# Kernel optimization log

Measured on AMD Instinct MI355X. Metric: run time of the kernel, lower is better.

## Reference

```python
import jax, jax.numpy as jnp
import numpy as np

C = 256

def setup_inputs() -> dict:
    key = jax.random.key(0)
    ks = jax.random.split(key, 8)
    B, H, W = 4, 64, 64
    x = jax.random.normal(ks[0], (B, C, H, W), dtype=jnp.float32)
    # 1x1 conv weights ~ kaiming uniform; bias zero
    bound = np.sqrt(6.0 / C)
    Wq = jax.random.uniform(ks[1], (C, C), minval=-bound, maxval=bound, dtype=jnp.float32)
    Wk = jax.random.uniform(ks[2], (C, C), minval=-bound, maxval=bound, dtype=jnp.float32)
    Wv = jax.random.uniform(ks[3], (C, C), minval=-bound, maxval=bound, dtype=jnp.float32)
    bq = jnp.zeros((C,), jnp.float32)
    bk = jnp.zeros((C,), jnp.float32)
    bv = jnp.zeros((C,), jnp.float32)
    # gamma initialized to zero in torch; use small nonzero so output depends on attn path
    gamma = jnp.array([0.1], dtype=jnp.float32)
    return {"x": x, "Wq": Wq, "bq": bq, "Wk": Wk, "bk": bk, "Wv": Wv, "bv": bv, "gamma": gamma}


def reference(x, Wq, bq, Wk, bk, Wv, bv, gamma):
    B, Cc, H, W = x.shape
    N = H * W
    xf = x.reshape(B, Cc, N)  # [B,C,N]
    # 1x1 conv == per-pixel linear over channels: out[b,o,n] = sum_c W[o,c]*x[b,c,n] + b[o]
    q = jnp.einsum('oc,bcn->bon', Wq, xf) + bq[None, :, None]  # [B,C,N]
    k = jnp.einsum('oc,bcn->bon', Wk, xf) + bk[None, :, None]
    v = jnp.einsum('oc,bcn->bon', Wv, xf) + bv[None, :, None]
    # energy[b,i,j] = q[b,:,i] . k[b,:,j]  (no scaling, as in source)
    energy = jnp.einsum('bci,bcj->bij', q, k)  # [B,N,N]
    attention = jax.nn.softmax(energy, axis=-1)
    # out[b,c,i] = sum_j v[b,c,j] * attention[b,i,j]  (bmm(value, attn^T))
    out = jnp.einsum('bcj,bij->bci', v, attention)
    out = out.reshape(B, Cc, H, W)
    return gamma * out + x
```

## Files before the change

### kernel.cpp

```cpp
#include <hip/hip_runtime.h>
#include <hip/hip_bf16.h>
#include <cstdint>


#define C_DIM 256
#define N_DIM 4096
#define B_DIM 4

typedef _Float16 f16;
typedef f16 f16x8 __attribute__((ext_vector_type(8)));
typedef f16 f16x4 __attribute__((ext_vector_type(4)));
typedef float f32x4 __attribute__((ext_vector_type(4)));

__device__ __forceinline__ void dma16(const f16* g, f16* l) {
  __builtin_amdgcn_global_load_lds(
      (const __attribute__((address_space(1))) unsigned int*)g,
      (__attribute__((address_space(3))) unsigned int*)l, 16, 0, 0);
}

__global__ __launch_bounds__(256) void k_prep_xs(const float* __restrict__ x,
                                                 f16* __restrict__ xs) {
  __shared__ float tile[64][65];
  const int b = blockIdx.z, nb = blockIdx.x * 64, cb = blockIdx.y * 64;
  const float* xb = x + (size_t)b * C_DIM * N_DIM;
  for (int i = threadIdx.x; i < 64 * 64; i += 256) {
    int c = i >> 6, n = i & 63;
    tile[c][n] = xb[(size_t)(cb + c) * N_DIM + nb + n];
  }
  __syncthreads();
  f16* xsb = xs + (size_t)b * N_DIM * C_DIM;
  for (int i = threadIdx.x; i < 64 * 64; i += 256) {
    int n = i >> 6, c = i & 63;
    xsb[(size_t)(nb + n) * C_DIM + cb + c] = (f16)tile[c][n];
  }
}

__global__ __launch_bounds__(256) void k_cast_w(const float* __restrict__ Wq,
                                                const float* __restrict__ Wk,
                                                const float* __restrict__ Wv,
                                                f16* __restrict__ Wh) {
  int i = blockIdx.x * 256 + threadIdx.x;
  int sel = i >> 16, j = i & 65535;
  const float* s = (sel == 0) ? Wq : (sel == 1) ? Wk : Wv;
  Wh[i] = (f16)s[j];
}

__global__ __launch_bounds__(256) void k_proj(const f16* __restrict__ xs,
                                              const f16* __restrict__ Wh,
                                              const float* __restrict__ bq,
                                              const float* __restrict__ bk,
                                              const float* __restrict__ bv,
                                              f16* __restrict__ Qh,
                                              f16* __restrict__ Kh,
                                              f16* __restrict__ Vh) {
  const int z = blockIdx.y;
  const int w = threadIdx.x >> 6, lane = threadIdx.x & 63;
  const int quad = lane >> 4, li = lane & 15;
  const f16* W = Wh + (size_t)z * 65536;
  const float* bias = (z == 0) ? bq : (z == 1) ? bk : bv;

  if (z < 2) {
    f16* out = (z == 0) ? Qh : Kh;
    const int g0 = (blockIdx.x * 4 + w) * 16;
    f16x8 a[8];
    const f16* arow = xs + (size_t)(g0 + li) * C_DIM + quad * 8;
#pragma unroll
    for (int kf = 0; kf < 8; kf++) a[kf] = *(const f16x8*)(arow + kf * 32);
    for (int ot = 0; ot < 16; ot++) {
      f32x4 acc = {0.f, 0.f, 0.f, 0.f};
      const f16* brow = W + (size_t)(ot * 16 + li) * C_DIM + quad * 8;
#pragma unroll
      for (int kf = 0; kf < 8; kf++) {
        f16x8 bf = *(const f16x8*)(brow + kf * 32);
        acc = __builtin_amdgcn_mfma_f32_16x16x32_f16(a[kf], bf, acc, 0, 0, 0);
      }
      float bb = bias[ot * 16 + li];
      f16* orow = out + (size_t)g0 * C_DIM + ot * 16 + li;
#pragma unroll
      for (int r = 0; r < 4; r++)
        orow[(size_t)(quad * 4 + r) * C_DIM] = (f16)(acc[r] + bb);
    }
  } else {
    const int t = blockIdx.x * 4 + w;
    const int b = t >> 8, j0 = (t & 255) * 16;
    f16x8 bfr[8];
    const f16* brow = xs + (size_t)(b * N_DIM + j0 + li) * C_DIM + quad * 8;
#pragma unroll
    for (int kf = 0; kf < 8; kf++) bfr[kf] = *(const f16x8*)(brow + kf * 32);
    for (int ot = 0; ot < 16; ot++) {
      f32x4 acc = {0.f, 0.f, 0.f, 0.f};
      const f16* arow = W + (size_t)(ot * 16 + li) * C_DIM + quad * 8;
#pragma unroll
      for (int kf = 0; kf < 8; kf++) {
        f16x8 af = *(const f16x8*)(arow + kf * 32);
        acc = __builtin_amdgcn_mfma_f32_16x16x32_f16(af, bfr[kf], acc, 0, 0, 0);
      }
      f16* obase = Vh + ((size_t)(b * C_DIM + ot * 16 + quad * 4)) * N_DIM + j0 + li;
#pragma unroll
      for (int r = 0; r < 4; r++) {
        float bb = bias[ot * 16 + quad * 4 + r];
        obase[(size_t)r * N_DIM] = (f16)(acc[r] + bb);
      }
    }
  }
}

#define JT 64
#define NT (N_DIM / JT)
#define KBUF 16896
#define VBUF 16896
#define K0_OFF 0
#define K1_OFF 16896
#define V0_OFF 33792
#define V1_OFF 50688
#define P_OFF  67584
#define PSTR 80
#define SMEM_F16 72704

__global__ __launch_bounds__(256, 1) void k_attn(const f16* __restrict__ Qh,
                                                 const f16* __restrict__ Kh,
                                                 const f16* __restrict__ Vh,
                                                 const float* __restrict__ x,
                                                 const float* __restrict__ gamma_p,
                                                 float* __restrict__ out) {
  __shared__ __align__(16) f16 smem[SMEM_F16];
  const int b = blockIdx.y;
  const int tid = threadIdx.x;
  const int w = tid >> 6, lane = tid & 63;
  const int quad = lane >> 4, li = lane & 15;
  const int ibase = blockIdx.x * 64 + w * 16;

  f16x8 qf[8];
  {
    const f16* qrow = Qh + (size_t)(b * N_DIM + ibase + li) * C_DIM + quad * 8;
#pragma unroll
    for (int kf = 0; kf < 8; kf++) qf[kf] = *(const f16x8*)(qrow + kf * 32);
  }
  const f16* Kb = Kh + (size_t)b * N_DIM * C_DIM;
  const f16* Vb = Vh + (size_t)b * C_DIM * N_DIM;
  f16* Pw = smem + P_OFF + w * 16 * PSTR;

  const float LOG2E = 1.4426950408889634f;
  float m = -3.0e38f, l = 0.0f;
  f32x4 acc[16];
#pragma unroll
  for (int ct = 0; ct < 16; ct++) acc[ct] = (f32x4){0.f, 0.f, 0.f, 0.f};

  {
    const f16* kg = Kb;
    const f16* vg = Vb;
#pragma unroll
    for (int it = 0; it < 8; it++) {
      int p = w * 8 + it;
      dma16(kg + (size_t)(2 * p + (lane >> 5)) * C_DIM + (lane & 31) * 8,
            smem + K0_OFF + p * 528);
      dma16(vg + (size_t)(p * 8 + (lane >> 3)) * N_DIM + (lane & 7) * 8,
            smem + V0_OFF + p * 528);
    }
  }
  __syncthreads();

  for (int t = 0; t < NT; t++) {
    const f16* Kc = smem + ((t & 1) ? K1_OFF : K0_OFF);
    const f16* Vc = smem + ((t & 1) ? V1_OFF : V0_OFF);

    if (t + 1 < NT) {
      f16* Kn = smem + ((t & 1) ? K0_OFF : K1_OFF);
      f16* Vn = smem + ((t & 1) ? V0_OFF : V1_OFF);
      const int jt = (t + 1) * JT;
      const f16* kg = Kb + (size_t)jt * C_DIM;
      const f16* vg = Vb + jt;
#pragma unroll
      for (int it = 0; it < 8; it++) {
        int p = w * 8 + it;
        dma16(kg + (size_t)(2 * p + (lane >> 5)) * C_DIM + (lane & 31) * 8,
              Kn + p * 528);
        dma16(vg + (size_t)(p * 8 + (lane >> 3)) * N_DIM + (lane & 7) * 8,
              Vn + p * 528);
      }
    }

    f32x4 s[4];
#pragma unroll
    for (int sub = 0; sub < 4; sub++) {
      f32x4 ss = {0.f, 0.f, 0.f, 0.f};
      const int r = sub * 16 + li;
      const f16* krow = Kc + (r >> 1) * 528 + (r & 1) * 256 + quad * 8;
#pragma unroll
      for (int kf = 0; kf < 8; kf++) {
        f16x8 kfr = *(const f16x8*)(krow + kf * 32);
        ss = __builtin_amdgcn_mfma_f32_16x16x32_f16(kfr, qf[kf], ss, 0, 0, 0);
      }
      s[sub] = ss;
    }

    float tm = -3.0e38f;
#pragma unroll
    for (int sub = 0; sub < 4; sub++)
      tm = fmaxf(tm, fmaxf(fmaxf(s[sub][0], s[sub][1]), fmaxf(s[sub][2], s[sub][3])));
    tm = fmaxf(tm, __shfl_xor(tm, 16));
    tm = fmaxf(tm, __shfl_xor(tm, 32));
    float nm = fmaxf(m, tm);
    float alpha = exp2f((m - nm) * LOG2E);
    m = nm;
    if (__any(alpha < 1.0f)) {
      l *= alpha;
#pragma unroll
      for (int ct = 0; ct < 16; ct++) {
        acc[ct][0] *= alpha; acc[ct][1] *= alpha;
        acc[ct][2] *= alpha; acc[ct][3] *= alpha;
      }
    }
#pragma unroll
    for (int sub = 0; sub < 4; sub++) {
      float p0 = exp2f((s[sub][0] - m) * LOG2E);
      float p1 = exp2f((s[sub][1] - m) * LOG2E);
      float p2 = exp2f((s[sub][2] - m) * LOG2E);
      float p3 = exp2f((s[sub][3] - m) * LOG2E);
      l += (p0 + p1) + (p2 + p3);
      *(f16x4*)(Pw + li * PSTR + sub * 16 + quad * 4) =
          (f16x4){(f16)p0, (f16)p1, (f16)p2, (f16)p3};
    }

    f16x8 pf0 = *(const f16x8*)(Pw + li * PSTR + quad * 8);
    f16x8 pf1 = *(const f16x8*)(Pw + li * PSTR + 32 + quad * 8);
#pragma unroll
    for (int ct = 0; ct < 16; ct++) {
      const f16* vrow = Vc + (ct * 2 + (li >> 3)) * 528 + (li & 7) * 64 + quad * 8;
      f16x8 v0 = *(const f16x8*)(vrow);
      f16x8 v1 = *(const f16x8*)(vrow + 32);
      acc[ct] = __builtin_amdgcn_mfma_f32_16x16x32_f16(v0, pf0, acc[ct], 0, 0, 0);
      acc[ct] = __builtin_amdgcn_mfma_f32_16x16x32_f16(v1, pf1, acc[ct], 0, 0, 0);
    }

    __syncthreads();
  }

  l += __shfl_xor(l, 16);
  l += __shfl_xor(l, 32);
  const float scale = gamma_p[0] / l;

  const float* xb = x + (size_t)b * C_DIM * N_DIM;
  float* ob = out + (size_t)b * C_DIM * N_DIM;
  const int icol = ibase + li;
#pragma unroll
  for (int ct = 0; ct < 16; ct++) {
#pragma unroll
    for (int r = 0; r < 4; r++) {
      size_t off = (size_t)(ct * 16 + quad * 4 + r) * N_DIM + icol;
      ob[off] = acc[ct][r] * scale + xb[off];
    }
  }
}

extern "C" void kernel_launch(void* const* d_in, const int* in_sizes, int n_in,
                              void* d_out, int out_size, void* d_ws, size_t ws_size,
                              hipStream_t stream) {
  const float* x     = (const float*)d_in[0];
  const float* Wq    = (const float*)d_in[1];
  const float* bq    = (const float*)d_in[2];
  const float* Wk    = (const float*)d_in[3];
  const float* bk    = (const float*)d_in[4];
  const float* Wv    = (const float*)d_in[5];
  const float* bv    = (const float*)d_in[6];
  const float* gamma = (const float*)d_in[7];
  float* out = (float*)d_out;

  char* ws = (char*)d_ws;
  f16* xs = (f16*)(ws);
  f16* Qh = (f16*)(ws + (size_t)8  * 1024 * 1024);
  f16* Kh = (f16*)(ws + (size_t)16 * 1024 * 1024);
  f16* Vh = (f16*)(ws + (size_t)24 * 1024 * 1024);
  f16* Wh = (f16*)(ws + (size_t)32 * 1024 * 1024);

  k_prep_xs<<<dim3(64, 4, 4), 256, 0, stream>>>(x, xs);
  k_cast_w<<<dim3(768), 256, 0, stream>>>(Wq, Wk, Wv, Wh);
  k_proj<<<dim3(256, 3), 256, 0, stream>>>(xs, Wh, bq, bk, bv, Qh, Kh, Vh);
  k_attn<<<dim3(64, 4), 256, 0, stream>>>(Qh, Kh, Vh, x, gamma, out);
}
```

Before: 299.5 us.

## Repartition attention work: warps split key rows for QK and channels for PV

```diff
diff --git a/kernel.cpp b/kernel.cpp
--- a/kernel.cpp
+++ b/kernel.cpp
@@ -107,15 +107,14 @@
 
 #define JT 64
 #define NT (N_DIM / JT)
-#define KBUF 16896
-#define VBUF 16896
 #define K0_OFF 0
 #define K1_OFF 16896
 #define V0_OFF 33792
 #define V1_OFF 50688
 #define P_OFF  67584
-#define PSTR 80
-#define SMEM_F16 72704
+#define PSTR 72
+#define MX_OFF 72192
+#define SMEM_F16 73216
 
 __global__ __launch_bounds__(256, 1) void k_attn(const f16* __restrict__ Qh,
                                                  const f16* __restrict__ Kh,
@@ -128,35 +127,36 @@
   const int tid = threadIdx.x;
   const int w = tid >> 6, lane = tid & 63;
   const int quad = lane >> 4, li = lane & 15;
-  const int ibase = blockIdx.x * 64 + w * 16;
-
-  f16x8 qf[8];
-  {
-    const f16* qrow = Qh + (size_t)(b * N_DIM + ibase + li) * C_DIM + quad * 8;
-#pragma unroll
-    for (int kf = 0; kf < 8; kf++) qf[kf] = *(const f16x8*)(qrow + kf * 32);
-  }
+  const int qg0 = blockIdx.x * 64;
+
   const f16* Kb = Kh + (size_t)b * N_DIM * C_DIM;
   const f16* Vb = Vh + (size_t)b * C_DIM * N_DIM;
-  f16* Pw = smem + P_OFF + w * 16 * PSTR;
-
-  const float LOG2E = 1.4426950408889634f;
-  float m = -3.0e38f, l = 0.0f;
-  f32x4 acc[16];
-#pragma unroll
-  for (int ct = 0; ct < 16; ct++) acc[ct] = (f32x4){0.f, 0.f, 0.f, 0.f};
-
-  {
-    const f16* kg = Kb;
-    const f16* vg = Vb;
-#pragma unroll
-    for (int it = 0; it < 8; it++) {
-      int p = w * 8 + it;
-      dma16(kg + (size_t)(2 * p + (lane >> 5)) * C_DIM + (lane & 31) * 8,
-            smem + K0_OFF + p * 528);
-      dma16(vg + (size_t)(p * 8 + (lane >> 3)) * N_DIM + (lane & 7) * 8,
-            smem + V0_OFF + p * 528);
-    }
+  float* mx = (float*)(smem + MX_OFF);
+  f16* Pq = smem + P_OFF;
+
+  f16x8 qf[4][8];
+#pragma unroll
+  for (int cb = 0; cb < 4; cb++) {
+    const f16* qrow = Qh + (size_t)(b * N_DIM + qg0 + cb * 16 + li) * C_DIM + quad * 8;
+#pragma unroll
+    for (int kf = 0; kf < 8; kf++) qf[cb][kf] = *(const f16x8*)(qrow + kf * 32);
+  }
+
+  float m[4] = {-3.0e38f, -3.0e38f, -3.0e38f, -3.0e38f};
+  float l[4] = {0.f, 0.f, 0.f, 0.f};
+  f32x4 acc[4][4];
+#pragma unroll
+  for (int a = 0; a < 4; a++)
+#pragma unroll
+    for (int c = 0; c < 4; c++) acc[a][c] = (f32x4){0.f, 0.f, 0.f, 0.f};
+
+#pragma unroll
+  for (int it = 0; it < 8; it++) {
+    int p = w * 8 + it;
+    dma16(Kb + (size_t)(2 * p + (lane >> 5)) * C_DIM + (lane & 31) * 8,
+          smem + K0_OFF + p * 528);
+    dma16(Vb + (size_t)(p * 8 + (lane >> 3)) * N_DIM + (lane & 7) * 8,
+          smem + V0_OFF + p * 528);
   }
   __syncthreads();
 
@@ -164,12 +164,42 @@
     const f16* Kc = smem + ((t & 1) ? K1_OFF : K0_OFF);
     const f16* Vc = smem + ((t & 1) ? V1_OFF : V0_OFF);
 
+    f16x8 kfr[8];
+    {
+      const int r = w * 16 + li;
+      const f16* krow = Kc + (r >> 1) * 528 + (r & 1) * 256 + quad * 8;
+#pragma unroll
+      for (int kf = 0; kf < 8; kf++) kfr[kf] = *(const f16x8*)(krow + kf * 32);
+    }
+    f32x4 s[4];
+#pragma unroll
+    for (int cb = 0; cb < 4; cb++) {
+      f32x4 ss = {0.f, 0.f, 0.f, 0.f};
+#pragma unroll
+      for (int kf = 0; kf < 8; kf++)
+        ss = __builtin_amdgcn_mfma_f32_16x16x32_f16(kfr[kf], qf[cb][kf], ss, 0, 0, 0);
+      s[cb] = ss;
+    }
+
+    float tmw[4];
+#pragma unroll
+    for (int cb = 0; cb < 4; cb++) {
+      float tm = fmaxf(fmaxf(s[cb][0], s[cb][1]), fmaxf(s[cb][2], s[cb][3]));
+      tm = fmaxf(tm, __shfl_xor(tm, 16));
+      tm = fmaxf(tm, __shfl_xor(tm, 32));
+      tmw[cb] = tm;
+    }
+    if (lane < 16) {
+#pragma unroll
+      for (int cb = 0; cb < 4; cb++) mx[(cb * 16 + lane) * 4 + w] = tmw[cb];
+    }
+    __syncthreads();
+
     if (t + 1 < NT) {
       f16* Kn = smem + ((t & 1) ? K0_OFF : K1_OFF);
       f16* Vn = smem + ((t & 1) ? V0_OFF : V1_OFF);
-      const int jt = (t + 1) * JT;
-      const f16* kg = Kb + (size_t)jt * C_DIM;
-      const f16* vg = Vb + jt;
+      const f16* kg = Kb + (size_t)(t + 1) * JT * C_DIM;
+      const f16* vg = Vb + (t + 1) * JT;
 #pragma unroll
       for (int it = 0; it < 8; it++) {
         int p = w * 8 + it;
@@ -180,75 +210,86 @@
       }
     }
 
-    f32x4 s[4];
-#pragma unroll
-    for (int sub = 0; sub < 4; sub++) {
-      f32x4 ss = {0.f, 0.f, 0.f, 0.f};
-      const int r = sub * 16 + li;
-      const f16* krow = Kc + (r >> 1) * 528 + (r & 1) * 256 + quad * 8;
-#pragma unroll
-      for (int kf = 0; kf < 8; kf++) {
-        f16x8 kfr = *(const f16x8*)(krow + kf * 32);
-        ss = __builtin_amdgcn_mfma_f32_16x16x32_f16(kfr, qf[kf], ss, 0, 0, 0);
-      }
-      s[sub] = ss;
-    }
-
-    float tm = -3.0e38f;
-#pragma unroll
-    for (int sub = 0; sub < 4; sub++)
-      tm = fmaxf(tm, fmaxf(fmaxf(s[sub][0], s[sub][1]), fmaxf(s[sub][2], s[sub][3])));
-    tm = fmaxf(tm, __shfl_xor(tm, 16));
-    tm = fmaxf(tm, __shfl_xor(tm, 32));
-    float nm = fmaxf(m, tm);
-    float alpha = exp2f((m - nm) * LOG2E);
-    m = nm;
-    if (__any(alpha < 1.0f)) {
-      l *= alpha;
-#pragma unroll
-      for (int ct = 0; ct < 16; ct++) {
-        acc[ct][0] *= alpha; acc[ct][1] *= alpha;
-        acc[ct][2] *= alpha; acc[ct][3] *= alpha;
-      }
-    }
-#pragma unroll
-    for (int sub = 0; sub < 4; sub++) {
-      float p0 = exp2f((s[sub][0] - m) * LOG2E);
-      float p1 = exp2f((s[sub][1] - m) * LOG2E);
-      float p2 = exp2f((s[sub][2] - m) * LOG2E);
-      float p3 = exp2f((s[sub][3] - m) * LOG2E);
-      l += (p0 + p1) + (p2 + p3);
-      *(f16x4*)(Pw + li * PSTR + sub * 16 + quad * 4) =
+    float nm[4], al[4];
+    bool need = false;
+#pragma unroll
+    for (int cb = 0; cb < 4; cb++) {
+      float4 mm = *(const float4*)&mx[(cb * 16 + li) * 4];
+      float bm = fmaxf(fmaxf(mm.x, mm.y), fmaxf(mm.z, mm.w));
+      nm[cb] = fmaxf(m[cb], bm);
+      al[cb] = __expf(m[cb] - nm[cb]);
+      need |= (nm[cb] > m[cb]);
+      m[cb] = nm[cb];
+    }
+    if (__any(need)) {
+#pragma unroll
+      for (int cb = 0; cb < 4; cb++) {
+        l[cb] *= al[cb];
+#pragma unroll
+        for (int ctb = 0; ctb < 4; ctb++) acc[ctb][cb] *= al[cb];
+      }
+    }
+#pragma unroll
+    for (int cb = 0; cb < 4; cb++) {
+      float p0 = __expf(s[cb][0] - m[cb]);
+      float p1 = __expf(s[cb][1] - m[cb]);
+      float p2 = __expf(s[cb][2] - m[cb]);
+      float p3 = __expf(s[cb][3] - m[cb]);
+      l[cb] += (p0 + p1) + (p2 + p3);
+      *(f16x4*)(Pq + (cb * 16 + li) * PSTR + w * 16 + quad * 4) =
           (f16x4){(f16)p0, (f16)p1, (f16)p2, (f16)p3};
     }
-
-    f16x8 pf0 = *(const f16x8*)(Pw + li * PSTR + quad * 8);
-    f16x8 pf1 = *(const f16x8*)(Pw + li * PSTR + 32 + quad * 8);
-#pragma unroll
-    for (int ct = 0; ct < 16; ct++) {
-      const f16* vrow = Vc + (ct * 2 + (li >> 3)) * 528 + (li & 7) * 64 + quad * 8;
-      f16x8 v0 = *(const f16x8*)(vrow);
-      f16x8 v1 = *(const f16x8*)(vrow + 32);
-      acc[ct] = __builtin_amdgcn_mfma_f32_16x16x32_f16(v0, pf0, acc[ct], 0, 0, 0);
-      acc[ct] = __builtin_amdgcn_mfma_f32_16x16x32_f16(v1, pf1, acc[ct], 0, 0, 0);
-    }
-
     __syncthreads();
-  }
-
-  l += __shfl_xor(l, 16);
-  l += __shfl_xor(l, 32);
-  const float scale = gamma_p[0] / l;
+
+#pragma unroll
+    for (int kf2 = 0; kf2 < 2; kf2++) {
+      f16x8 vf[4];
+#pragma unroll
+      for (int ctb = 0; ctb < 4; ctb++) {
+        int c = w * 64 + ctb * 16 + li;
+        vf[ctb] = *(const f16x8*)(Vc + (c >> 3) * 528 + (c & 7) * 64 + kf2 * 32 + quad * 8);
+      }
+#pragma unroll
+      for (int cb = 0; cb < 4; cb++) {
+        f16x8 pf = *(const f16x8*)(Pq + (cb * 16 + li) * PSTR + kf2 * 32 + quad * 8);
+#pragma unroll
+        for (int ctb = 0; ctb < 4; ctb++)
+          acc[ctb][cb] = __builtin_amdgcn_mfma_f32_16x16x32_f16(vf[ctb], pf, acc[ctb][cb], 0, 0, 0);
+      }
+    }
+  }
+
+#pragma unroll
+  for (int cb = 0; cb < 4; cb++) {
+    l[cb] += __shfl_xor(l[cb], 16);
+    l[cb] += __shfl_xor(l[cb], 32);
+  }
+  __syncthreads();
+  if (lane < 16) {
+#pragma unroll
+    for (int cb = 0; cb < 4; cb++) mx[(cb * 16 + lane) * 4 + w] = l[cb];
+  }
+  __syncthreads();
+  const float g = gamma_p[0];
+  float scale[4];
+#pragma unroll
+  for (int cb = 0; cb < 4; cb++) {
+    float4 ll = *(const float4*)&mx[(cb * 16 + li) * 4];
+    scale[cb] = g / (((ll.x + ll.y) + (ll.z + ll.w)));
+  }
 
   const float* xb = x + (size_t)b * C_DIM * N_DIM;
   float* ob = out + (size_t)b * C_DIM * N_DIM;
-  const int icol = ibase + li;
-#pragma unroll
-  for (int ct = 0; ct < 16; ct++) {
+#pragma unroll
+  for (int ctb = 0; ctb < 4; ctb++) {
 #pragma unroll
     for (int r = 0; r < 4; r++) {
-      size_t off = (size_t)(ct * 16 + quad * 4 + r) * N_DIM + icol;
-      ob[off] = acc[ct][r] * scale + xb[off];
+      int ch = w * 64 + ctb * 16 + quad * 4 + r;
+#pragma unroll
+      for (int cb = 0; cb < 4; cb++) {
+        size_t off = (size_t)ch * N_DIM + qg0 + cb * 16 + li;
+        ob[off] = acc[ctb][cb][r] * scale[cb] + xb[off];
+      }
     }
   }
 }
```

Result: no change. 302.9 us (+1.1%).

## Split attention work across waves by key half and channel slice with smaller tiles

Applied to the files above, without the earlier changes.

```diff
diff --git a/kernel.cpp b/kernel.cpp
--- a/kernel.cpp
+++ b/kernel.cpp
@@ -105,19 +105,19 @@
   }
 }
 
-#define JT 64
+#define Q_BLK 32
+#define JT 32
 #define NT (N_DIM / JT)
-#define KBUF 16896
-#define VBUF 16896
 #define K0_OFF 0
-#define K1_OFF 16896
-#define V0_OFF 33792
-#define V1_OFF 50688
-#define P_OFF  67584
-#define PSTR 80
-#define SMEM_F16 72704
-
-__global__ __launch_bounds__(256, 1) void k_attn(const f16* __restrict__ Qh,
+#define K1_OFF 8448
+#define V0_OFF 16896
+#define V1_OFF 25216
+#define P_OFF  33536
+#define MX_OFF 34816
+#define PSTR 40
+#define SMEM_F16 34944
+
+__global__ __launch_bounds__(256, 2) void k_attn(const f16* __restrict__ Qh,
                                                  const f16* __restrict__ Kh,
                                                  const f16* __restrict__ Vh,
                                                  const float* __restrict__ x,
@@ -128,35 +128,38 @@
   const int tid = threadIdx.x;
   const int w = tid >> 6, lane = tid & 63;
   const int quad = lane >> 4, li = lane & 15;
-  const int ibase = blockIdx.x * 64 + w * 16;
+  const int q0 = blockIdx.x * Q_BLK;
+  const int qg = w >> 1;
+  const int kg = w & 1;
+  float* mx = (float*)(smem + MX_OFF);
+  f16* Pq = smem + P_OFF;
 
   f16x8 qf[8];
   {
-    const f16* qrow = Qh + (size_t)(b * N_DIM + ibase + li) * C_DIM + quad * 8;
+    const f16* qrow = Qh + (size_t)(b * N_DIM + q0 + qg * 16 + li) * C_DIM + quad * 8;
 #pragma unroll
     for (int kf = 0; kf < 8; kf++) qf[kf] = *(const f16x8*)(qrow + kf * 32);
   }
   const f16* Kb = Kh + (size_t)b * N_DIM * C_DIM;
   const f16* Vb = Vh + (size_t)b * C_DIM * N_DIM;
-  f16* Pw = smem + P_OFF + w * 16 * PSTR;
+
+  const int kland = lane * 8;
+  const size_t vland = (size_t)(lane >> 2) * N_DIM + (lane & 3) * 8;
 
   const float LOG2E = 1.4426950408889634f;
-  float m = -3.0e38f, l = 0.0f;
-  f32x4 acc[16];
-#pragma unroll
-  for (int ct = 0; ct < 16; ct++) acc[ct] = (f32x4){0.f, 0.f, 0.f, 0.f};
-
-  {
-    const f16* kg = Kb;
-    const f16* vg = Vb;
-#pragma unroll
-    for (int it = 0; it < 8; it++) {
-      int p = w * 8 + it;
-      dma16(kg + (size_t)(2 * p + (lane >> 5)) * C_DIM + (lane & 31) * 8,
-            smem + K0_OFF + p * 528);
-      dma16(vg + (size_t)(p * 8 + (lane >> 3)) * N_DIM + (lane & 7) * 8,
-            smem + V0_OFF + p * 528);
-    }
+  float m[2] = {-3.0e38f, -3.0e38f};
+  float l_lane = 0.0f;
+  f32x4 acc[4][2];
+#pragma unroll
+  for (int a = 0; a < 4; a++)
+#pragma unroll
+    for (int c = 0; c < 2; c++) acc[a][c] = (f32x4){0.f, 0.f, 0.f, 0.f};
+
+#pragma unroll
+  for (int i = 0; i < 4; i++) {
+    int p = w * 4 + i;
+    dma16(Kb + p * 512 + kland, smem + K0_OFF + p * 528 + kland);
+    dma16(Vb + (size_t)(p * 16) * N_DIM + vland, smem + V0_OFF + p * 520 + kland);
   }
   __syncthreads();
 
@@ -164,91 +167,105 @@
     const f16* Kc = smem + ((t & 1) ? K1_OFF : K0_OFF);
     const f16* Vc = smem + ((t & 1) ? V1_OFF : V0_OFF);
 
+    f32x4 s = {0.f, 0.f, 0.f, 0.f};
+    {
+      const int r = kg * 16 + li;
+      const f16* krow = Kc + (r >> 1) * 528 + (r & 1) * 256 + quad * 8;
+#pragma unroll
+      for (int kf = 0; kf < 8; kf++) {
+        f16x8 kfr = *(const f16x8*)(krow + kf * 32);
+        s = __builtin_amdgcn_mfma_f32_16x16x32_f16(kfr, qf[kf], s, 0, 0, 0);
+      }
+    }
+
+    float pm = fmaxf(fmaxf(s[0], s[1]), fmaxf(s[2], s[3]));
+    pm = fmaxf(pm, __shfl_xor(pm, 16));
+    pm = fmaxf(pm, __shfl_xor(pm, 32));
+    if (lane < 16) mx[(qg * 16 + lane) * 2 + kg] = pm;
+    __syncthreads();
+
     if (t + 1 < NT) {
       f16* Kn = smem + ((t & 1) ? K0_OFF : K1_OFF);
       f16* Vn = smem + ((t & 1) ? V0_OFF : V1_OFF);
-      const int jt = (t + 1) * JT;
-      const f16* kg = Kb + (size_t)jt * C_DIM;
-      const f16* vg = Vb + jt;
-#pragma unroll
-      for (int it = 0; it < 8; it++) {
-        int p = w * 8 + it;
-        dma16(kg + (size_t)(2 * p + (lane >> 5)) * C_DIM + (lane & 31) * 8,
-              Kn + p * 528);
-        dma16(vg + (size_t)(p * 8 + (lane >> 3)) * N_DIM + (lane & 7) * 8,
-              Vn + p * 528);
-      }
-    }
-
-    f32x4 s[4];
-#pragma unroll
-    for (int sub = 0; sub < 4; sub++) {
-      f32x4 ss = {0.f, 0.f, 0.f, 0.f};
-      const int r = sub * 16 + li;
-      const f16* krow = Kc + (r >> 1) * 528 + (r & 1) * 256 + quad * 8;
-#pragma unroll
-      for (int kf = 0; kf < 8; kf++) {
-        f16x8 kfr = *(const f16x8*)(krow + kf * 32);
-        ss = __builtin_amdgcn_mfma_f32_16x16x32_f16(kfr, qf[kf], ss, 0, 0, 0);
-      }
-      s[sub] = ss;
-    }
-
-    float tm = -3.0e38f;
-#pragma unroll
-    for (int sub = 0; sub < 4; sub++)
-      tm = fmaxf(tm, fmaxf(fmaxf(s[sub][0], s[sub][1]), fmaxf(s[sub][2], s[sub][3])));
-    tm = fmaxf(tm, __shfl_xor(tm, 16));
-    tm = fmaxf(tm, __shfl_xor(tm, 32));
-    float nm = fmaxf(m, tm);
-    float alpha = exp2f((m - nm) * LOG2E);
-    m = nm;
-    if (__any(alpha < 1.0f)) {
-      l *= alpha;
-#pragma unroll
-      for (int ct = 0; ct < 16; ct++) {
-        acc[ct][0] *= alpha; acc[ct][1] *= alpha;
-        acc[ct][2] *= alpha; acc[ct][3] *= alpha;
-      }
-    }
-#pragma unroll
-    for (int sub = 0; sub < 4; sub++) {
-      float p0 = exp2f((s[sub][0] - m) * LOG2E);
-      float p1 = exp2f((s[sub][1] - m) * LOG2E);
-      float p2 = exp2f((s[sub][2] - m) * LOG2E);
-      float p3 = exp2f((s[sub][3] - m) * LOG2E);
-      l += (p0 + p1) + (p2 + p3);
-      *(f16x4*)(Pw + li * PSTR + sub * 16 + quad * 4) =
+      const f16* kg_p = Kb + (size_t)(t + 1) * (JT * C_DIM);
+      const f16* vg_p = Vb + (t + 1) * JT;
+#pragma unroll
+      for (int i = 0; i < 4; i++) {
+        int p = w * 4 + i;
+        dma16(kg_p + p * 512 + kland, Kn + p * 528 + kland);
+        dma16(vg_p + (size_t)(p * 16) * N_DIM + vland, Vn + p * 520 + kland);
+      }
+    }
+
+    float al[2];
+    bool need = false;
+#pragma unroll
+    for (int cb = 0; cb < 2; cb++) {
+      float2 mm = *(const float2*)&mx[(cb * 16 + li) * 2];
+      float bm = fmaxf(mm.x, mm.y);
+      float nm = fmaxf(m[cb], bm);
+      al[cb] = __expf(m[cb] - nm);
+      need |= (nm > m[cb]);
+      m[cb] = nm;
+    }
+    if (__any(need)) {
+      l_lane *= al[qg];
+#pragma unroll
+      for (int ct = 0; ct < 4; ct++) {
+#pragma unroll
+        for (int cb = 0; cb < 2; cb++) acc[ct][cb] *= al[cb];
+      }
+    }
+
+    {
+      float p0 = __expf(s[0] - m[qg]);
+      float p1 = __expf(s[1] - m[qg]);
+      float p2 = __expf(s[2] - m[qg]);
+      float p3 = __expf(s[3] - m[qg]);
+      l_lane += (p0 + p1) + (p2 + p3);
+      *(f16x4*)(Pq + (qg * 16 + li) * PSTR + kg * 16 + quad * 4) =
           (f16x4){(f16)p0, (f16)p1, (f16)p2, (f16)p3};
     }
-
-    f16x8 pf0 = *(const f16x8*)(Pw + li * PSTR + quad * 8);
-    f16x8 pf1 = *(const f16x8*)(Pw + li * PSTR + 32 + quad * 8);
-#pragma unroll
-    for (int ct = 0; ct < 16; ct++) {
-      const f16* vrow = Vc + (ct * 2 + (li >> 3)) * 528 + (li & 7) * 64 + quad * 8;
-      f16x8 v0 = *(const f16x8*)(vrow);
-      f16x8 v1 = *(const f16x8*)(vrow + 32);
-      acc[ct] = __builtin_amdgcn_mfma_f32_16x16x32_f16(v0, pf0, acc[ct], 0, 0, 0);
-      acc[ct] = __builtin_amdgcn_mfma_f32_16x16x32_f16(v1, pf1, acc[ct], 0, 0, 0);
-    }
-
     __syncthreads();
-  }
-
-  l += __shfl_xor(l, 16);
-  l += __shfl_xor(l, 32);
-  const float scale = gamma_p[0] / l;
+
+    f16x8 pf[2];
+#pragma unroll
+    for (int cb = 0; cb < 2; cb++)
+      pf[cb] = *(const f16x8*)(Pq + (cb * 16 + li) * PSTR + quad * 8);
+#pragma unroll
+    for (int ct = 0; ct < 4; ct++) {
+      f16x8 vf = *(const f16x8*)(Vc + (w * 4 + ct) * 520 + li * 32 + quad * 8);
+#pragma unroll
+      for (int cb = 0; cb < 2; cb++)
+        acc[ct][cb] = __builtin_amdgcn_mfma_f32_16x16x32_f16(vf, pf[cb], acc[ct][cb], 0, 0, 0);
+    }
+  }
+
+  l_lane += __shfl_xor(l_lane, 16);
+  l_lane += __shfl_xor(l_lane, 32);
+  __syncthreads();
+  if (lane < 16) mx[(qg * 16 + lane) * 2 + kg] = l_lane;
+  __syncthreads();
+  const float g = gamma_p[0];
+  float scale[2];
+#pragma unroll
+  for (int cb = 0; cb < 2; cb++) {
+    float2 ll = *(const float2*)&mx[(cb * 16 + li) * 2];
+    scale[cb] = g / (ll.x + ll.y);
+  }
 
   const float* xb = x + (size_t)b * C_DIM * N_DIM;
   float* ob = out + (size_t)b * C_DIM * N_DIM;
-  const int icol = ibase + li;
-#pragma unroll
-  for (int ct = 0; ct < 16; ct++) {
+#pragma unroll
+  for (int ct = 0; ct < 4; ct++) {
 #pragma unroll
     for (int r = 0; r < 4; r++) {
-      size_t off = (size_t)(ct * 16 + quad * 4 + r) * N_DIM + icol;
-      ob[off] = acc[ct][r] * scale + xb[off];
+      int ch = w * 64 + ct * 16 + quad * 4 + r;
+#pragma unroll
+      for (int cb = 0; cb < 2; cb++) {
+        size_t off = (size_t)ch * N_DIM + q0 + cb * 16 + li;
+        ob[off] = acc[ct][cb][r] * scale[cb] + xb[off];
+      }
     }
   }
 }
@@ -276,5 +293,5 @@
   k_prep_xs<<<dim3(64, 4, 4), 256, 0, stream>>>(x, xs);
   k_cast_w<<<dim3(768), 256, 0, stream>>>(Wq, Wk, Wv, Wh);
   k_proj<<<dim3(256, 3), 256, 0, stream>>>(xs, Wh, bq, bk, bv, Qh, Kh, Vh);
-  k_attn<<<dim3(64, 4), 256, 0, stream>>>(Qh, Kh, Vh, x, gamma, out);
-}
+  k_attn<<<dim3(128, 4), 256, 0, stream>>>(Qh, Kh, Vh, x, gamma, out);
+}
```

Measured after the change: 307.6 us. 2.7% more time.

## Restructure attention to 32x32 MFMA with split-KV warp pairs and merged softmax

Applied to the files above, without the earlier changes.

```diff
diff --git a/kernel.cpp b/kernel.cpp
--- a/kernel.cpp
+++ b/kernel.cpp
@@ -11,6 +11,7 @@
 typedef f16 f16x8 __attribute__((ext_vector_type(8)));
 typedef f16 f16x4 __attribute__((ext_vector_type(4)));
 typedef float f32x4 __attribute__((ext_vector_type(4)));
+typedef float f32x16 __attribute__((ext_vector_type(16)));
 
 __device__ __forceinline__ void dma16(const f16* g, f16* l) {
   __builtin_amdgcn_global_load_lds(
@@ -105,16 +106,12 @@
   }
 }
 
-#define JT 64
-#define NT (N_DIM / JT)
-#define KBUF 16896
-#define VBUF 16896
-#define K0_OFF 0
-#define K1_OFF 16896
-#define V0_OFF 33792
-#define V1_OFF 50688
+#define JT 32
+#define NPER 64
+#define KB_OFF 0
+#define VB_OFF 33792
 #define P_OFF  67584
-#define PSTR 80
+#define PSTR 40
 #define SMEM_F16 72704
 
 __global__ __launch_bounds__(256, 1) void k_attn(const f16* __restrict__ Qh,
@@ -127,128 +124,167 @@
   const int b = blockIdx.y;
   const int tid = threadIdx.x;
   const int w = tid >> 6, lane = tid & 63;
-  const int quad = lane >> 4, li = lane & 15;
-  const int ibase = blockIdx.x * 64 + w * 16;
-
-  f16x8 qf[8];
-  {
-    const f16* qrow = Qh + (size_t)(b * N_DIM + ibase + li) * C_DIM + quad * 8;
-#pragma unroll
-    for (int kf = 0; kf < 8; kf++) qf[kf] = *(const f16x8*)(qrow + kf * 32);
-  }
+  const int cq = lane & 31;
+  const int h = lane >> 5;
+  const int qs = w >> 1, par = w & 1;
+  const int sp = w >> 1, kind = w & 1;
+  const int q0 = blockIdx.x * 64;
+
   const f16* Kb = Kh + (size_t)b * N_DIM * C_DIM;
   const f16* Vb = Vh + (size_t)b * C_DIM * N_DIM;
-  f16* Pw = smem + P_OFF + w * 16 * PSTR;
-
-  const float LOG2E = 1.4426950408889634f;
-  float m = -3.0e38f, l = 0.0f;
-  f32x4 acc[16];
-#pragma unroll
-  for (int ct = 0; ct < 16; ct++) acc[ct] = (f32x4){0.f, 0.f, 0.f, 0.f};
-
+  f16* Pw = smem + P_OFF + w * 1280;
+
+  f16x8 qf[16];
   {
-    const f16* kg = Kb;
-    const f16* vg = Vb;
-#pragma unroll
-    for (int it = 0; it < 8; it++) {
-      int p = w * 8 + it;
-      dma16(kg + (size_t)(2 * p + (lane >> 5)) * C_DIM + (lane & 31) * 8,
-            smem + K0_OFF + p * 528);
-      dma16(vg + (size_t)(p * 8 + (lane >> 3)) * N_DIM + (lane & 7) * 8,
-            smem + V0_OFF + p * 528);
+    const f16* qrow = Qh + (size_t)(b * N_DIM + q0 + qs * 32 + cq) * C_DIM + h * 8;
+#pragma unroll
+    for (int c = 0; c < 16; c++) qf[c] = *(const f16x8*)(qrow + c * 16);
+  }
+
+  float m = -3.0e38f, l_lane = 0.0f;
+  f32x16 acc[8];
+#pragma unroll
+  for (int ct = 0; ct < 8; ct++) acc[ct] = (f32x16){};
+
+  {
+    const int kt = sp * JT;
+    if (kind == 0) {
+      f16* dst = smem + KB_OFF + (sp * 2 + 0) * 8448;
+      const int c8 = (lane & 31) * 8;
+#pragma unroll
+      for (int i = 0; i < 16; i++)
+        dma16(Kb + (size_t)(kt + 2 * i + h) * C_DIM + c8, dst + i * 528);
+    } else {
+      f16* dst = smem + VB_OFF + (sp * 2 + 0) * 8448;
+#pragma unroll
+      for (int i = 0; i < 16; i++)
+        dma16(Vb + (size_t)(i * 16 + (lane >> 2)) * N_DIM + kt + (lane & 3) * 8,
+              dst + i * 528);
     }
   }
   __syncthreads();
 
-  for (int t = 0; t < NT; t++) {
-    const f16* Kc = smem + ((t & 1) ? K1_OFF : K0_OFF);
-    const f16* Vc = smem + ((t & 1) ? V1_OFF : V0_OFF);
-
-    if (t + 1 < NT) {
-      f16* Kn = smem + ((t & 1) ? K0_OFF : K1_OFF);
-      f16* Vn = smem + ((t & 1) ? V0_OFF : V1_OFF);
-      const int jt = (t + 1) * JT;
-      const f16* kg = Kb + (size_t)jt * C_DIM;
-      const f16* vg = Vb + jt;
-#pragma unroll
-      for (int it = 0; it < 8; it++) {
-        int p = w * 8 + it;
-        dma16(kg + (size_t)(2 * p + (lane >> 5)) * C_DIM + (lane & 31) * 8,
-              Kn + p * 528);
-        dma16(vg + (size_t)(p * 8 + (lane >> 3)) * N_DIM + (lane & 7) * 8,
-              Vn + p * 528);
+  for (int u = 0; u < NPER; u++) {
+    const int db = u & 1;
+    const f16* Kc = smem + KB_OFF + (par * 2 + db) * 8448;
+    const f16* Vc = smem + VB_OFF + (par * 2 + db) * 8448;
+
+    f32x16 s0 = (f32x16){}, s1 = (f32x16){};
+    {
+      const f16* ka = Kc + (cq >> 1) * 528 + (cq & 1) * 256 + h * 8;
+#pragma unroll
+      for (int c = 0; c < 8; c++)
+        s0 = __builtin_amdgcn_mfma_f32_32x32x16_f16(*(const f16x8*)(ka + c * 16),
+                                                    qf[c], s0, 0, 0, 0);
+#pragma unroll
+      for (int c = 8; c < 16; c++)
+        s1 = __builtin_amdgcn_mfma_f32_32x32x16_f16(*(const f16x8*)(ka + c * 16),
+                                                    qf[c], s1, 0, 0, 0);
+    }
+    f32x16 s = s0 + s1;
+
+    if (u + 1 < NPER) {
+      const int db2 = db ^ 1;
+      const int kt = (2 * (u + 1) + sp) * JT;
+      if (kind == 0) {
+        f16* dst = smem + KB_OFF + (sp * 2 + db2) * 8448;
+        const int c8 = (lane & 31) * 8;
+#pragma unroll
+        for (int i = 0; i < 16; i++)
+          dma16(Kb + (size_t)(kt + 2 * i + h) * C_DIM + c8, dst + i * 528);
+      } else {
+        f16* dst = smem + VB_OFF + (sp * 2 + db2) * 8448;
+#pragma unroll
+        for (int i = 0; i < 16; i++)
+          dma16(Vb + (size_t)(i * 16 + (lane >> 2)) * N_DIM + kt + (lane & 3) * 8,
+                dst + i * 528);
       }
     }
 
-    f32x4 s[4];
-#pragma unroll
-    for (int sub = 0; sub < 4; sub++) {
-      f32x4 ss = {0.f, 0.f, 0.f, 0.f};
-      const int r = sub * 16 + li;
-      const f16* krow = Kc + (r >> 1) * 528 + (r & 1) * 256 + quad * 8;
-#pragma unroll
-      for (int kf = 0; kf < 8; kf++) {
-        f16x8 kfr = *(const f16x8*)(krow + kf * 32);
-        ss = __builtin_amdgcn_mfma_f32_16x16x32_f16(kfr, qf[kf], ss, 0, 0, 0);
-      }
-      s[sub] = ss;
-    }
-
-    float tm = -3.0e38f;
-#pragma unroll
-    for (int sub = 0; sub < 4; sub++)
-      tm = fmaxf(tm, fmaxf(fmaxf(s[sub][0], s[sub][1]), fmaxf(s[sub][2], s[sub][3])));
-    tm = fmaxf(tm, __shfl_xor(tm, 16));
+    float tm = s[0];
+#pragma unroll
+    for (int i = 1; i < 16; i++) tm = fmaxf(tm, s[i]);
     tm = fmaxf(tm, __shfl_xor(tm, 32));
     float nm = fmaxf(m, tm);
-    float alpha = exp2f((m - nm) * LOG2E);
+    float al = __expf(m - nm);
+    bool upd = nm > m;
     m = nm;
-    if (__any(alpha < 1.0f)) {
-      l *= alpha;
-#pragma unroll
-      for (int ct = 0; ct < 16; ct++) {
-        acc[ct][0] *= alpha; acc[ct][1] *= alpha;
-        acc[ct][2] *= alpha; acc[ct][3] *= alpha;
-      }
-    }
-#pragma unroll
-    for (int sub = 0; sub < 4; sub++) {
-      float p0 = exp2f((s[sub][0] - m) * LOG2E);
-      float p1 = exp2f((s[sub][1] - m) * LOG2E);
-      float p2 = exp2f((s[sub][2] - m) * LOG2E);
-      float p3 = exp2f((s[sub][3] - m) * LOG2E);
-      l += (p0 + p1) + (p2 + p3);
-      *(f16x4*)(Pw + li * PSTR + sub * 16 + quad * 4) =
+    if (__any(upd)) {
+      l_lane *= al;
+#pragma unroll
+      for (int ct = 0; ct < 8; ct++) acc[ct] *= al;
+    }
+    float lsum = 0.0f;
+#pragma unroll
+    for (int rq = 0; rq < 4; rq++) {
+      float p0 = __expf(s[rq * 4 + 0] - m);
+      float p1 = __expf(s[rq * 4 + 1] - m);
+      float p2 = __expf(s[rq * 4 + 2] - m);
+      float p3 = __expf(s[rq * 4 + 3] - m);
+      lsum += (p0 + p1) + (p2 + p3);
+      *(f16x4*)(Pw + cq * PSTR + rq * 8 + 4 * h) =
           (f16x4){(f16)p0, (f16)p1, (f16)p2, (f16)p3};
     }
-
-    f16x8 pf0 = *(const f16x8*)(Pw + li * PSTR + quad * 8);
-    f16x8 pf1 = *(const f16x8*)(Pw + li * PSTR + 32 + quad * 8);
-#pragma unroll
-    for (int ct = 0; ct < 16; ct++) {
-      const f16* vrow = Vc + (ct * 2 + (li >> 3)) * 528 + (li & 7) * 64 + quad * 8;
-      f16x8 v0 = *(const f16x8*)(vrow);
-      f16x8 v1 = *(const f16x8*)(vrow + 32);
-      acc[ct] = __builtin_amdgcn_mfma_f32_16x16x32_f16(v0, pf0, acc[ct], 0, 0, 0);
-      acc[ct] = __builtin_amdgcn_mfma_f32_16x16x32_f16(v1, pf1, acc[ct], 0, 0, 0);
+    l_lane += lsum;
+
+    f16x8 pf0 = *(const f16x8*)(Pw + cq * PSTR + h * 8);
+    f16x8 pf1 = *(const f16x8*)(Pw + cq * PSTR + 16 + h * 8);
+#pragma unroll
+    for (int ct = 0; ct < 8; ct++) {
+      const f16* va = Vc + (ct * 2 + (cq >> 4)) * 528 + (cq & 15) * 32 + h * 8;
+      acc[ct] = __builtin_amdgcn_mfma_f32_32x32x16_f16(*(const f16x8*)(va), pf0,
+                                                       acc[ct], 0, 0, 0);
+      acc[ct] = __builtin_amdgcn_mfma_f32_32x32x16_f16(*(const f16x8*)(va + 16), pf1,
+                                                       acc[ct], 0, 0, 0);
     }
 
     __syncthreads();
   }
 
-  l += __shfl_xor(l, 16);
-  l += __shfl_xor(l, 32);
-  const float scale = gamma_p[0] / l;
+  l_lane += __shfl_xor(l_lane, 32);
+  float* xch = (float*)smem;
+  float* mlx = xch + 16384;
+  {
+    const int sct0 = (w & 1) ? 0 : 4;
+    float* myr = xch + w * 4096;
+#pragma unroll
+    for (int t2 = 0; t2 < 4; t2++)
+#pragma unroll
+      for (int i = 0; i < 8; i++)
+        *(float2*)(myr + (t2 * 8 + i) * 128 + lane * 2) =
+            make_float2(acc[sct0 + t2][2 * i], acc[sct0 + t2][2 * i + 1]);
+    mlx[w * 128 + lane] = m;
+    mlx[512 + w * 128 + lane] = l_lane;
+  }
+  __syncthreads();
+  const int partner = w ^ 1;
+  const int kct0 = (w & 1) ? 4 : 0;
+  float mp = mlx[partner * 128 + lane];
+  float lp = mlx[512 + partner * 128 + lane];
+  float ms = fmaxf(m, mp);
+  float a0 = __expf(m - ms), a1 = __expf(mp - ms);
+  float ls = a0 * l_lane + a1 * lp;
+  const float scale = gamma_p[0] / ls;
+  const float* pr = xch + partner * 4096;
 
   const float* xb = x + (size_t)b * C_DIM * N_DIM;
   float* ob = out + (size_t)b * C_DIM * N_DIM;
-  const int icol = ibase + li;
-#pragma unroll
-  for (int ct = 0; ct < 16; ct++) {
-#pragma unroll
-    for (int r = 0; r < 4; r++) {
-      size_t off = (size_t)(ct * 16 + quad * 4 + r) * N_DIM + icol;
-      ob[off] = acc[ct][r] * scale + xb[off];
+  const int qcol = q0 + qs * 32 + cq;
+#pragma unroll
+  for (int t2 = 0; t2 < 4; t2++) {
+    const int ct = kct0 + t2;
+#pragma unroll
+    for (int i = 0; i < 8; i++) {
+      float2 o = *(const float2*)(pr + (t2 * 8 + i) * 128 + lane * 2);
+      float v0 = a0 * acc[ct][2 * i] + a1 * o.x;
+      float v1 = a0 * acc[ct][2 * i + 1] + a1 * o.y;
+      int r0 = 2 * i, r1 = 2 * i + 1;
+      int ch0 = ct * 32 + (r0 & 3) + 8 * (r0 >> 2) + 4 * h;
+      int ch1 = ct * 32 + (r1 & 3) + 8 * (r1 >> 2) + 4 * h;
+      size_t off0 = (size_t)ch0 * N_DIM + qcol;
+      size_t off1 = (size_t)ch1 * N_DIM + qcol;
+      ob[off0] = v0 * scale + xb[off0];
+      ob[off1] = v1 * scale + xb[off1];
     }
   }
 }
```

Measured after the change: 495.1 us. +65.3%, slower.
